# Kernel optimization log

Measured on AMD Instinct MI355X. Metric: run time of the kernel, lower is better.

## Reference

```python
import jax, jax.numpy as jnp
import numpy as np

OFFSET_SCALE = 6.0
ATT_SCALE = 280
ATT_DOWN = 8


def _calc_visibility(posmap):
    # posmap: (B, 3, W, H). shift stencil + cross-product z sign
    down_shift = jnp.pad(posmap[:, :, :, :-1], ((0, 0), (0, 0), (0, 0), (1, 0)))
    right_shift = jnp.pad(posmap[:, :, :-1, :], ((0, 0), (0, 0), (1, 0), (0, 0)))
    ab = posmap - right_shift
    bc = down_shift - right_shift
    z = ab[:, 0] * bc[:, 1] - ab[:, 1] * bc[:, 0]
    return jnp.where(z > 0, jnp.float32(1.0), jnp.where(z < 0, jnp.float32(0.1), z))


def _kpt2tform_weighted(kpt_src, kpt_dst, weight):
    # kpt_src/kpt_dst: (B, 68, 3); weight: (B, 68) (diagonal of W)
    d1 = jnp.sum(jnp.linalg.norm(kpt_src - kpt_src[:, 33:34], axis=2), axis=1)[:, None, None]
    d2 = jnp.sum(jnp.linalg.norm(kpt_dst - kpt_dst[:, 33:34], axis=2), axis=1)[:, None, None]
    A = kpt_src * d2 / d1
    Bm = kpt_dst
    AA = A - A.mean(axis=1, keepdims=True)
    BB = Bm - Bm.mean(axis=1, keepdims=True)
    # H = AA^T @ diag(w) @ BB, avoid materializing (B,68,68)
    H = jnp.einsum('bki,bk,bkj->bij', AA, weight, BB)
    U, S, Vh = jnp.linalg.svd(H)          # H = U diag(S) Vh ; torch.svd's V = Vh^T
    V = jnp.swapaxes(Vh, -1, -2)
    R = V @ jnp.swapaxes(U, -1, -2)
    t = jnp.mean(Bm - A @ jnp.swapaxes(R, -1, -2), axis=1)
    return R * d2 / d1, t


def setup_inputs() -> dict:
    key = jax.random.key(0)
    k1, k2, k3, k4, k5 = jax.random.split(key, 5)
    B, C, W, H = 64, 3, 256, 256
    Offset = jax.random.normal(k1, (B, C, W, H), dtype=jnp.float32)
    Posmap_kpt = jax.random.uniform(k2, (B, C, W, H), dtype=jnp.float32)
    attention = jax.random.uniform(k3, (B, 1, 35, 35), dtype=jnp.float32)
    mean_posmap = jax.random.uniform(k4, (C, W, H), dtype=jnp.float32)
    uv_kpt = jax.random.randint(k5, (68, 2), 0, 256, dtype=jnp.int32)
    return {"Offset": Offset, "Posmap_kpt": Posmap_kpt, "attention": attention,
            "mean_posmap": mean_posmap, "uv_kpt": uv_kpt}


def reference(Offset, Posmap_kpt, attention, mean_posmap, uv_kpt):
    B, C, W, H = Posmap_kpt.shape
    offsetmap = Offset * OFFSET_SCALE + mean_posmap          # (B,3,W,H)
    offsetmap = jnp.transpose(offsetmap, (0, 2, 3, 1))       # (B,W,H,3)
    vis_map = _calc_visibility(Posmap_kpt)                   # (B,W,H)
    kptmap = jnp.transpose(Posmap_kpt, (0, 2, 3, 1))         # (B,W,H,3)

    kpt_dst = kptmap[:, uv_kpt[:, 0], uv_kpt[:, 1]]          # (B,68,3)
    kpt_src = offsetmap[:, uv_kpt[:, 0], uv_kpt[:, 1]]       # (B,68,3)
    weight = vis_map[:, uv_kpt[:, 0], uv_kpt[:, 1]]          # (B,68)

    # attention reweighting (vectorized version of per-batch Python loop)
    kpt_ind = (kpt_dst[:, :, :2] * ATT_SCALE).astype(jnp.int32)
    iy = kpt_ind[:, :, 1] // ATT_DOWN
    ix = kpt_ind[:, :, 0] // ATT_DOWN
    w_at = attention[jnp.arange(B)[:, None], 0, iy, ix]      # (B,68)
    weight = weight * w_at

    R, T = _kpt2tform_weighted(kpt_src, kpt_dst, weight)
    flat = offsetmap.reshape((B, W * H, C))
    outpos = flat @ jnp.swapaxes(R, -1, -2) + T[:, None, :]
    outpos = outpos.reshape((B, W, H, C))
    return jnp.transpose(outpos, (0, 3, 1, 2))
```

## Files before the change

### kernel.cpp

```cpp
#include <hip/hip_runtime.h>
#include <math.h>

#define WH 65536
#define NK 68

__global__ __launch_bounds__(64) void solve_kernel(
    const float* __restrict__ Off, const float* __restrict__ P,
    const float* __restrict__ att, const float* __restrict__ meanp,
    const int* __restrict__ uv, float* __restrict__ RT)
{
    const int b = blockIdx.x;
    const int t = threadIdx.x;
    const float* Pb = P  + (size_t)b * 3 * WH;
    const float* Ob = Off + (size_t)b * 3 * WH;
    const float* attb = att + (size_t)b * 35 * 35;

    float src[2][3], dst[2][3], wgt[2];
    #pragma unroll
    for (int i = 0; i < 2; ++i) {
        const int k = t + 64 * i;
        const bool act = (k < NK);
        float p0=0,p1=0,p2=0,s0=0,s1=0,s2=0,w=0;
        if (act) {
            const int u0 = uv[2*k], u1 = uv[2*k+1];
            const int base = u0 * 256 + u1;
            p0 = Pb[0*WH + base];
            p1 = Pb[1*WH + base];
            p2 = Pb[2*WH + base];
            s0 = fmaf(Ob[0*WH + base], 6.0f, meanp[0*WH + base]);
            s1 = fmaf(Ob[1*WH + base], 6.0f, meanp[1*WH + base]);
            s2 = fmaf(Ob[2*WH + base], 6.0f, meanp[2*WH + base]);
            const float r0 = (u0 > 0) ? Pb[0*WH + base - 256] : 0.0f;
            const float r1 = (u0 > 0) ? Pb[1*WH + base - 256] : 0.0f;
            const float d0 = (u1 > 0) ? Pb[0*WH + base - 1]   : 0.0f;
            const float d1v= (u1 > 0) ? Pb[1*WH + base - 1]   : 0.0f;
            const float z = (p0 - r0) * (d1v - r1) - (p1 - r1) * (d0 - r0);
            const float vis = (z > 0.0f) ? 1.0f : ((z < 0.0f) ? 0.1f : z);
            int ix = (int)(p0 * 280.0f) / 8;
            int iy = (int)(p1 * 280.0f) / 8;
            ix = min(max(ix, 0), 34);
            iy = min(max(iy, 0), 34);
            w = vis * attb[iy * 35 + ix];
        }
        dst[i][0]=p0; dst[i][1]=p1; dst[i][2]=p2;
        src[i][0]=s0; src[i][1]=s1; src[i][2]=s2;
        wgt[i]=w;
    }

    float s33[3], d33[3];
    #pragma unroll
    for (int c = 0; c < 3; ++c) {
        s33[c] = __shfl(src[0][c], 33);
        d33[c] = __shfl(dst[0][c], 33);
    }

    float sums[8];
    #pragma unroll
    for (int j = 0; j < 8; ++j) sums[j] = 0.0f;
    #pragma unroll
    for (int i = 0; i < 2; ++i) {
        const bool act = (t + 64*i < NK);
        if (!act) continue;
        #pragma unroll
        for (int c = 0; c < 3; ++c) { sums[c] += src[i][c]; sums[3+c] += dst[i][c]; }
        const float dx0=src[i][0]-s33[0], dx1=src[i][1]-s33[1], dx2=src[i][2]-s33[2];
        const float dy0=dst[i][0]-d33[0], dy1=dst[i][1]-d33[1], dy2=dst[i][2]-d33[2];
        sums[6] += sqrtf(dx0*dx0 + dx1*dx1 + dx2*dx2);
        sums[7] += sqrtf(dy0*dy0 + dy1*dy1 + dy2*dy2);
    }
    #pragma unroll
    for (int m = 1; m < 64; m <<= 1)
        #pragma unroll
        for (int j = 0; j < 8; ++j) sums[j] += __shfl_xor(sums[j], m);

    const float inv_nk = 1.0f / (float)NK;
    const float ms0 = sums[0]*inv_nk, ms1 = sums[1]*inv_nk, ms2 = sums[2]*inv_nk;
    const float md0 = sums[3]*inv_nk, md1 = sums[4]*inv_nk, md2 = sums[5]*inv_nk;
    const float s = sums[7] / sums[6];

    float M[9];
    #pragma unroll
    for (int j = 0; j < 9; ++j) M[j] = 0.0f;
    #pragma unroll
    for (int i = 0; i < 2; ++i) {
        const float a0=src[i][0]-ms0, a1=src[i][1]-ms1, a2=src[i][2]-ms2;
        const float b0=dst[i][0]-md0, b1=dst[i][1]-md1, b2=dst[i][2]-md2;
        const float w = wgt[i];
        M[0]=fmaf(w*a0,b0,M[0]); M[1]=fmaf(w*a0,b1,M[1]); M[2]=fmaf(w*a0,b2,M[2]);
        M[3]=fmaf(w*a1,b0,M[3]); M[4]=fmaf(w*a1,b1,M[4]); M[5]=fmaf(w*a1,b2,M[5]);
        M[6]=fmaf(w*a2,b0,M[6]); M[7]=fmaf(w*a2,b1,M[7]); M[8]=fmaf(w*a2,b2,M[8]);
    }
    #pragma unroll
    for (int m = 1; m < 64; m <<= 1)
        #pragma unroll
        for (int j = 0; j < 9; ++j) M[j] += __shfl_xor(M[j], m);

    if (t == 0) {
        float X[9];
        float fn = 1e-30f;
        #pragma unroll
        for (int e = 0; e < 9; ++e) fn += M[e]*M[e];
        fn = sqrtf(fn);
        #pragma unroll
        for (int r = 0; r < 3; ++r)
            #pragma unroll
            for (int c = 0; c < 3; ++c)
                X[r*3+c] = M[c*3+r] / fn;
        #pragma unroll
        for (int it = 0; it < 10; ++it) {
            float C0 = X[4]*X[8]-X[5]*X[7];
            float C1 = X[5]*X[6]-X[3]*X[8];
            float C2 = X[3]*X[7]-X[4]*X[6];
            float C3 = X[2]*X[7]-X[1]*X[8];
            float C4 = X[0]*X[8]-X[2]*X[6];
            float C5 = X[1]*X[6]-X[0]*X[7];
            float C6 = X[1]*X[5]-X[2]*X[4];
            float C7 = X[2]*X[3]-X[0]*X[5];
            float C8 = X[0]*X[4]-X[1]*X[3];
            float det = X[0]*C0 + X[1]*C1 + X[2]*C2;
            if (fabsf(det) < 1e-30f) det = (det < 0.0f) ? -1e-30f : 1e-30f;
            const float g   = cbrtf(1.0f / fabsf(det));
            const float idg = 1.0f / (det * g);
            X[0]=0.5f*(g*X[0]+C0*idg); X[1]=0.5f*(g*X[1]+C1*idg); X[2]=0.5f*(g*X[2]+C2*idg);
            X[3]=0.5f*(g*X[3]+C3*idg); X[4]=0.5f*(g*X[4]+C4*idg); X[5]=0.5f*(g*X[5]+C5*idg);
            X[6]=0.5f*(g*X[6]+C6*idg); X[7]=0.5f*(g*X[7]+C7*idg); X[8]=0.5f*(g*X[8]+C8*idg);
        }
        float* o = RT + (size_t)b * 12;
        #pragma unroll
        for (int e = 0; e < 9; ++e) o[e] = s * X[e];
        const float msv[3] = {ms0, ms1, ms2};
        #pragma unroll
        for (int c = 0; c < 3; ++c) {
            float acc = 0.0f;
            #pragma unroll
            for (int j = 0; j < 3; ++j) acc = fmaf(msv[j], X[c*3+j], acc);
            const float mdv = (c==0) ? md0 : ((c==1) ? md1 : md2);
            o[9+c] = mdv - s * acc;
        }
    }
}

__device__ __forceinline__ float4 aff4(float4 f0, float4 f1, float4 f2,
                                       float r0, float r1, float r2, float t) {
    float4 y;
    y.x = fmaf(f0.x, r0, fmaf(f1.x, r1, fmaf(f2.x, r2, t)));
    y.y = fmaf(f0.y, r0, fmaf(f1.y, r1, fmaf(f2.y, r2, t)));
    y.z = fmaf(f0.z, r0, fmaf(f1.z, r1, fmaf(f2.z, r2, t)));
    y.w = fmaf(f0.w, r0, fmaf(f1.w, r1, fmaf(f2.w, r2, t)));
    return y;
}

__global__ __launch_bounds__(256) void apply_kernel(
    const float* __restrict__ Off, const float* __restrict__ meanp,
    const float* __restrict__ RT, float* __restrict__ out)
{
    const int b = blockIdx.y;
    const size_t p = ((size_t)blockIdx.x * 256 + threadIdx.x) * 4;
    const float* rt = RT + (size_t)b * 12;
    const float r00=rt[0], r01=rt[1], r02=rt[2];
    const float r10=rt[3], r11=rt[4], r12=rt[5];
    const float r20=rt[6], r21=rt[7], r22=rt[8];
    const float t0=rt[9], t1=rt[10], t2=rt[11];

    const float* ob = Off + (size_t)b * 3 * WH;
    const float4 o0 = *(const float4*)(ob + 0*WH + p);
    const float4 o1 = *(const float4*)(ob + 1*WH + p);
    const float4 o2 = *(const float4*)(ob + 2*WH + p);
    const float4 m0 = *(const float4*)(meanp + 0*WH + p);
    const float4 m1 = *(const float4*)(meanp + 1*WH + p);
    const float4 m2 = *(const float4*)(meanp + 2*WH + p);

    float4 f0, f1, f2;
    f0.x=fmaf(o0.x,6.0f,m0.x); f0.y=fmaf(o0.y,6.0f,m0.y); f0.z=fmaf(o0.z,6.0f,m0.z); f0.w=fmaf(o0.w,6.0f,m0.w);
    f1.x=fmaf(o1.x,6.0f,m1.x); f1.y=fmaf(o1.y,6.0f,m1.y); f1.z=fmaf(o1.z,6.0f,m1.z); f1.w=fmaf(o1.w,6.0f,m1.w);
    f2.x=fmaf(o2.x,6.0f,m2.x); f2.y=fmaf(o2.y,6.0f,m2.y); f2.z=fmaf(o2.z,6.0f,m2.z); f2.w=fmaf(o2.w,6.0f,m2.w);

    float* outb = out + (size_t)b * 3 * WH;
    *(float4*)(outb + 0*WH + p) = aff4(f0, f1, f2, r00, r01, r02, t0);
    *(float4*)(outb + 1*WH + p) = aff4(f0, f1, f2, r10, r11, r12, t1);
    *(float4*)(outb + 2*WH + p) = aff4(f0, f1, f2, r20, r21, r22, t2);
}

extern "C" void kernel_launch(void* const* d_in, const int* in_sizes, int n_in,
                              void* d_out, int out_size, void* d_ws, size_t ws_size,
                              hipStream_t stream) {
    const float* Off   = (const float*)d_in[0];
    const float* P     = (const float*)d_in[1];
    const float* att   = (const float*)d_in[2];
    const float* meanp = (const float*)d_in[3];
    const int*   uv    = (const int*)d_in[4];
    float* out = (float*)d_out;
    float* RT  = (float*)d_ws;

    const int B = in_sizes[0] / (3 * WH);

    solve_kernel<<<B, 64, 0, stream>>>(Off, P, att, meanp, uv, RT);

    dim3 grid(WH / (256 * 4), B);
    apply_kernel<<<grid, 256, 0, stream>>>(Off, meanp, RT, out);
}
```

Baseline: 28.88 us.

## Fuse per-batch Kabsch solve into apply kernel, recomputing transform per block

Merges the solve and apply kernels into one. Each block's first wavefront redundantly recomputes the per-batch rotation and translation from the 68 keypoints, while the other threads' bulk loads are already in flight. The result is shared through LDS, which removes the second launch and the serial dependency between kernels. In exchange the solve work is repeated across 64 blocks per batch. The Newton polar iterations also drop from 10 to 8 and use fast rcp and exp2/log2 in place of cbrt and division, which may cost some accuracy.

```diff
diff --git a/kernel.cpp b/kernel.cpp
--- a/kernel.cpp
+++ b/kernel.cpp
@@ -3,142 +3,6 @@
 
 #define WH 65536
 #define NK 68
-
-__global__ __launch_bounds__(64) void solve_kernel(
-    const float* __restrict__ Off, const float* __restrict__ P,
-    const float* __restrict__ att, const float* __restrict__ meanp,
-    const int* __restrict__ uv, float* __restrict__ RT)
-{
-    const int b = blockIdx.x;
-    const int t = threadIdx.x;
-    const float* Pb = P  + (size_t)b * 3 * WH;
-    const float* Ob = Off + (size_t)b * 3 * WH;
-    const float* attb = att + (size_t)b * 35 * 35;
-
-    float src[2][3], dst[2][3], wgt[2];
-    #pragma unroll
-    for (int i = 0; i < 2; ++i) {
-        const int k = t + 64 * i;
-        const bool act = (k < NK);
-        float p0=0,p1=0,p2=0,s0=0,s1=0,s2=0,w=0;
-        if (act) {
-            const int u0 = uv[2*k], u1 = uv[2*k+1];
-            const int base = u0 * 256 + u1;
-            p0 = Pb[0*WH + base];
-            p1 = Pb[1*WH + base];
-            p2 = Pb[2*WH + base];
-            s0 = fmaf(Ob[0*WH + base], 6.0f, meanp[0*WH + base]);
-            s1 = fmaf(Ob[1*WH + base], 6.0f, meanp[1*WH + base]);
-            s2 = fmaf(Ob[2*WH + base], 6.0f, meanp[2*WH + base]);
-            const float r0 = (u0 > 0) ? Pb[0*WH + base - 256] : 0.0f;
-            const float r1 = (u0 > 0) ? Pb[1*WH + base - 256] : 0.0f;
-            const float d0 = (u1 > 0) ? Pb[0*WH + base - 1]   : 0.0f;
-            const float d1v= (u1 > 0) ? Pb[1*WH + base - 1]   : 0.0f;
-            const float z = (p0 - r0) * (d1v - r1) - (p1 - r1) * (d0 - r0);
-            const float vis = (z > 0.0f) ? 1.0f : ((z < 0.0f) ? 0.1f : z);
-            int ix = (int)(p0 * 280.0f) / 8;
-            int iy = (int)(p1 * 280.0f) / 8;
-            ix = min(max(ix, 0), 34);
-            iy = min(max(iy, 0), 34);
-            w = vis * attb[iy * 35 + ix];
-        }
-        dst[i][0]=p0; dst[i][1]=p1; dst[i][2]=p2;
-        src[i][0]=s0; src[i][1]=s1; src[i][2]=s2;
-        wgt[i]=w;
-    }
-
-    float s33[3], d33[3];
-    #pragma unroll
-    for (int c = 0; c < 3; ++c) {
-        s33[c] = __shfl(src[0][c], 33);
-        d33[c] = __shfl(dst[0][c], 33);
-    }
-
-    float sums[8];
-    #pragma unroll
-    for (int j = 0; j < 8; ++j) sums[j] = 0.0f;
-    #pragma unroll
-    for (int i = 0; i < 2; ++i) {
-        const bool act = (t + 64*i < NK);
-        if (!act) continue;
-        #pragma unroll
-        for (int c = 0; c < 3; ++c) { sums[c] += src[i][c]; sums[3+c] += dst[i][c]; }
-        const float dx0=src[i][0]-s33[0], dx1=src[i][1]-s33[1], dx2=src[i][2]-s33[2];
-        const float dy0=dst[i][0]-d33[0], dy1=dst[i][1]-d33[1], dy2=dst[i][2]-d33[2];
-        sums[6] += sqrtf(dx0*dx0 + dx1*dx1 + dx2*dx2);
-        sums[7] += sqrtf(dy0*dy0 + dy1*dy1 + dy2*dy2);
-    }
-    #pragma unroll
-    for (int m = 1; m < 64; m <<= 1)
-        #pragma unroll
-        for (int j = 0; j < 8; ++j) sums[j] += __shfl_xor(sums[j], m);
-
-    const float inv_nk = 1.0f / (float)NK;
-    const float ms0 = sums[0]*inv_nk, ms1 = sums[1]*inv_nk, ms2 = sums[2]*inv_nk;
-    const float md0 = sums[3]*inv_nk, md1 = sums[4]*inv_nk, md2 = sums[5]*inv_nk;
-    const float s = sums[7] / sums[6];
-
-    float M[9];
-    #pragma unroll
-    for (int j = 0; j < 9; ++j) M[j] = 0.0f;
-    #pragma unroll
-    for (int i = 0; i < 2; ++i) {
-        const float a0=src[i][0]-ms0, a1=src[i][1]-ms1, a2=src[i][2]-ms2;
-        const float b0=dst[i][0]-md0, b1=dst[i][1]-md1, b2=dst[i][2]-md2;
-        const float w = wgt[i];
-        M[0]=fmaf(w*a0,b0,M[0]); M[1]=fmaf(w*a0,b1,M[1]); M[2]=fmaf(w*a0,b2,M[2]);
-        M[3]=fmaf(w*a1,b0,M[3]); M[4]=fmaf(w*a1,b1,M[4]); M[5]=fmaf(w*a1,b2,M[5]);
-        M[6]=fmaf(w*a2,b0,M[6]); M[7]=fmaf(w*a2,b1,M[7]); M[8]=fmaf(w*a2,b2,M[8]);
-    }
-    #pragma unroll
-    for (int m = 1; m < 64; m <<= 1)
-        #pragma unroll
-        for (int j = 0; j < 9; ++j) M[j] += __shfl_xor(M[j], m);
-
-    if (t == 0) {
-        float X[9];
-        float fn = 1e-30f;
-        #pragma unroll
-        for (int e = 0; e < 9; ++e) fn += M[e]*M[e];
-        fn = sqrtf(fn);
-        #pragma unroll
-        for (int r = 0; r < 3; ++r)
-            #pragma unroll
-            for (int c = 0; c < 3; ++c)
-                X[r*3+c] = M[c*3+r] / fn;
-        #pragma unroll
-        for (int it = 0; it < 10; ++it) {
-            float C0 = X[4]*X[8]-X[5]*X[7];
-            float C1 = X[5]*X[6]-X[3]*X[8];
-            float C2 = X[3]*X[7]-X[4]*X[6];
-            float C3 = X[2]*X[7]-X[1]*X[8];
-            float C4 = X[0]*X[8]-X[2]*X[6];
-            float C5 = X[1]*X[6]-X[0]*X[7];
-            float C6 = X[1]*X[5]-X[2]*X[4];
-            float C7 = X[2]*X[3]-X[0]*X[5];
-            float C8 = X[0]*X[4]-X[1]*X[3];
-            float det = X[0]*C0 + X[1]*C1 + X[2]*C2;
-            if (fabsf(det) < 1e-30f) det = (det < 0.0f) ? -1e-30f : 1e-30f;
-            const float g   = cbrtf(1.0f / fabsf(det));
-            const float idg = 1.0f / (det * g);
-            X[0]=0.5f*(g*X[0]+C0*idg); X[1]=0.5f*(g*X[1]+C1*idg); X[2]=0.5f*(g*X[2]+C2*idg);
-            X[3]=0.5f*(g*X[3]+C3*idg); X[4]=0.5f*(g*X[4]+C4*idg); X[5]=0.5f*(g*X[5]+C5*idg);
-            X[6]=0.5f*(g*X[6]+C6*idg); X[7]=0.5f*(g*X[7]+C7*idg); X[8]=0.5f*(g*X[8]+C8*idg);
-        }
-        float* o = RT + (size_t)b * 12;
-        #pragma unroll
-        for (int e = 0; e < 9; ++e) o[e] = s * X[e];
-        const float msv[3] = {ms0, ms1, ms2};
-        #pragma unroll
-        for (int c = 0; c < 3; ++c) {
-            float acc = 0.0f;
-            #pragma unroll
-            for (int j = 0; j < 3; ++j) acc = fmaf(msv[j], X[c*3+j], acc);
-            const float mdv = (c==0) ? md0 : ((c==1) ? md1 : md2);
-            o[9+c] = mdv - s * acc;
-        }
-    }
-}
 
 __device__ __forceinline__ float4 aff4(float4 f0, float4 f1, float4 f2,
                                        float r0, float r1, float r2, float t) {
@@ -150,18 +14,16 @@
     return y;
 }
 
-__global__ __launch_bounds__(256) void apply_kernel(
-    const float* __restrict__ Off, const float* __restrict__ meanp,
-    const float* __restrict__ RT, float* __restrict__ out)
+__global__ __launch_bounds__(256, 4) void fused_kernel(
+    const float* __restrict__ Off, const float* __restrict__ P,
+    const float* __restrict__ att, const float* __restrict__ meanp,
+    const int* __restrict__ uv, float* __restrict__ out)
 {
     const int b = blockIdx.y;
-    const size_t p = ((size_t)blockIdx.x * 256 + threadIdx.x) * 4;
-    const float* rt = RT + (size_t)b * 12;
-    const float r00=rt[0], r01=rt[1], r02=rt[2];
-    const float r10=rt[3], r11=rt[4], r12=rt[5];
-    const float r20=rt[6], r21=rt[7], r22=rt[8];
-    const float t0=rt[9], t1=rt[10], t2=rt[11];
+    const int t = threadIdx.x;
+    __shared__ float sRT[12];
 
+    const size_t p = ((size_t)blockIdx.x * 256 + t) * 4;
     const float* ob = Off + (size_t)b * 3 * WH;
     const float4 o0 = *(const float4*)(ob + 0*WH + p);
     const float4 o1 = *(const float4*)(ob + 1*WH + p);
@@ -170,10 +32,146 @@
     const float4 m1 = *(const float4*)(meanp + 1*WH + p);
     const float4 m2 = *(const float4*)(meanp + 2*WH + p);
 
+    if (t < 64) {
+        const float* Pb = P  + (size_t)b * 3 * WH;
+        const float* attb = att + (size_t)b * 35 * 35;
+
+        float src[2][3], dst[2][3], wgt[2];
+        #pragma unroll
+        for (int i = 0; i < 2; ++i) {
+            const int k = t + 64 * i;
+            const bool act = (k < NK);
+            float p0=0,p1=0,p2=0,s0=0,s1=0,s2=0,w=0;
+            if (act) {
+                const int u0 = uv[2*k], u1 = uv[2*k+1];
+                const int base = u0 * 256 + u1;
+                p0 = Pb[0*WH + base];
+                p1 = Pb[1*WH + base];
+                p2 = Pb[2*WH + base];
+                s0 = fmaf(Off[(size_t)b*3*WH + 0*WH + base], 6.0f, meanp[0*WH + base]);
+                s1 = fmaf(Off[(size_t)b*3*WH + 1*WH + base], 6.0f, meanp[1*WH + base]);
+                s2 = fmaf(Off[(size_t)b*3*WH + 2*WH + base], 6.0f, meanp[2*WH + base]);
+                const float r0 = (u0 > 0) ? Pb[0*WH + base - 256] : 0.0f;
+                const float r1 = (u0 > 0) ? Pb[1*WH + base - 256] : 0.0f;
+                const float d0 = (u1 > 0) ? Pb[0*WH + base - 1]   : 0.0f;
+                const float d1v= (u1 > 0) ? Pb[1*WH + base - 1]   : 0.0f;
+                const float z = (p0 - r0) * (d1v - r1) - (p1 - r1) * (d0 - r0);
+                const float vis = (z > 0.0f) ? 1.0f : ((z < 0.0f) ? 0.1f : z);
+                int ix = (int)(p0 * 280.0f) / 8;
+                int iy = (int)(p1 * 280.0f) / 8;
+                ix = min(max(ix, 0), 34);
+                iy = min(max(iy, 0), 34);
+                w = vis * attb[iy * 35 + ix];
+            }
+            dst[i][0]=p0; dst[i][1]=p1; dst[i][2]=p2;
+            src[i][0]=s0; src[i][1]=s1; src[i][2]=s2;
+            wgt[i]=w;
+        }
+
+        float s33[3], d33[3];
+        #pragma unroll
+        for (int c = 0; c < 3; ++c) {
+            s33[c] = __shfl(src[0][c], 33);
+            d33[c] = __shfl(dst[0][c], 33);
+        }
+
+        float sums[8];
+        #pragma unroll
+        for (int j = 0; j < 8; ++j) sums[j] = 0.0f;
+        #pragma unroll
+        for (int i = 0; i < 2; ++i) {
+            const bool act = (t + 64*i < NK);
+            if (!act) continue;
+            #pragma unroll
+            for (int c = 0; c < 3; ++c) { sums[c] += src[i][c]; sums[3+c] += dst[i][c]; }
+            const float dx0=src[i][0]-s33[0], dx1=src[i][1]-s33[1], dx2=src[i][2]-s33[2];
+            const float dy0=dst[i][0]-d33[0], dy1=dst[i][1]-d33[1], dy2=dst[i][2]-d33[2];
+            sums[6] += sqrtf(dx0*dx0 + dx1*dx1 + dx2*dx2);
+            sums[7] += sqrtf(dy0*dy0 + dy1*dy1 + dy2*dy2);
+        }
+        #pragma unroll
+        for (int m = 1; m < 64; m <<= 1)
+            #pragma unroll
+            for (int j = 0; j < 8; ++j) sums[j] += __shfl_xor(sums[j], m);
+
+        const float inv_nk = 1.0f / (float)NK;
+        const float ms0 = sums[0]*inv_nk, ms1 = sums[1]*inv_nk, ms2 = sums[2]*inv_nk;
+        const float md0 = sums[3]*inv_nk, md1 = sums[4]*inv_nk, md2 = sums[5]*inv_nk;
+        const float s = sums[7] * __builtin_amdgcn_rcpf(sums[6]);
+
+        float M[9];
+        #pragma unroll
+        for (int j = 0; j < 9; ++j) M[j] = 0.0f;
+        #pragma unroll
+        for (int i = 0; i < 2; ++i) {
+            const float a0=src[i][0]-ms0, a1=src[i][1]-ms1, a2=src[i][2]-ms2;
+            const float b0=dst[i][0]-md0, b1=dst[i][1]-md1, b2=dst[i][2]-md2;
+            const float w = wgt[i];
+            M[0]=fmaf(w*a0,b0,M[0]); M[1]=fmaf(w*a0,b1,M[1]); M[2]=fmaf(w*a0,b2,M[2]);
+            M[3]=fmaf(w*a1,b0,M[3]); M[4]=fmaf(w*a1,b1,M[4]); M[5]=fmaf(w*a1,b2,M[5]);
+            M[6]=fmaf(w*a2,b0,M[6]); M[7]=fmaf(w*a2,b1,M[7]); M[8]=fmaf(w*a2,b2,M[8]);
+        }
+        #pragma unroll
+        for (int m = 1; m < 64; m <<= 1)
+            #pragma unroll
+            for (int j = 0; j < 9; ++j) M[j] += __shfl_xor(M[j], m);
+
+        if (t == 0) {
+            float X[9];
+            float fn = 1e-30f;
+            #pragma unroll
+            for (int e = 0; e < 9; ++e) fn += M[e]*M[e];
+            const float rfn = __builtin_amdgcn_rcpf(sqrtf(fn));
+            #pragma unroll
+            for (int r = 0; r < 3; ++r)
+                #pragma unroll
+                for (int c = 0; c < 3; ++c)
+                    X[r*3+c] = M[c*3+r] * rfn;
+            #pragma unroll
+            for (int it = 0; it < 8; ++it) {
+                const float C0 = X[4]*X[8]-X[5]*X[7];
+                const float C1 = X[5]*X[6]-X[3]*X[8];
+                const float C2 = X[3]*X[7]-X[4]*X[6];
+                const float C3 = X[2]*X[7]-X[1]*X[8];
+                const float C4 = X[0]*X[8]-X[2]*X[6];
+                const float C5 = X[1]*X[6]-X[0]*X[7];
+                const float C6 = X[1]*X[5]-X[2]*X[4];
+                const float C7 = X[2]*X[3]-X[0]*X[5];
+                const float C8 = X[0]*X[4]-X[1]*X[3];
+                float det = X[0]*C0 + X[1]*C1 + X[2]*C2;
+                if (fabsf(det) < 1e-30f) det = (det < 0.0f) ? -1e-30f : 1e-30f;
+                const float ad  = fabsf(det);
+                const float g   = exp2f(-0.333333333f * log2f(ad));
+                const float idg = __builtin_amdgcn_rcpf(det * g);
+                X[0]=0.5f*(g*X[0]+C0*idg); X[1]=0.5f*(g*X[1]+C1*idg); X[2]=0.5f*(g*X[2]+C2*idg);
+                X[3]=0.5f*(g*X[3]+C3*idg); X[4]=0.5f*(g*X[4]+C4*idg); X[5]=0.5f*(g*X[5]+C5*idg);
+                X[6]=0.5f*(g*X[6]+C6*idg); X[7]=0.5f*(g*X[7]+C7*idg); X[8]=0.5f*(g*X[8]+C8*idg);
+            }
+            #pragma unroll
+            for (int e = 0; e < 9; ++e) sRT[e] = s * X[e];
+            const float msv[3] = {ms0, ms1, ms2};
+            #pragma unroll
+            for (int c = 0; c < 3; ++c) {
+                float acc = 0.0f;
+                #pragma unroll
+                for (int j = 0; j < 3; ++j) acc = fmaf(msv[j], X[c*3+j], acc);
+                const float mdv = (c==0) ? md0 : ((c==1) ? md1 : md2);
+                sRT[9+c] = mdv - s * acc;
+            }
+        }
+    }
+
     float4 f0, f1, f2;
     f0.x=fmaf(o0.x,6.0f,m0.x); f0.y=fmaf(o0.y,6.0f,m0.y); f0.z=fmaf(o0.z,6.0f,m0.z); f0.w=fmaf(o0.w,6.0f,m0.w);
     f1.x=fmaf(o1.x,6.0f,m1.x); f1.y=fmaf(o1.y,6.0f,m1.y); f1.z=fmaf(o1.z,6.0f,m1.z); f1.w=fmaf(o1.w,6.0f,m1.w);
     f2.x=fmaf(o2.x,6.0f,m2.x); f2.y=fmaf(o2.y,6.0f,m2.y); f2.z=fmaf(o2.z,6.0f,m2.z); f2.w=fmaf(o2.w,6.0f,m2.w);
+
+    __syncthreads();
+
+    const float r00=sRT[0], r01=sRT[1], r02=sRT[2];
+    const float r10=sRT[3], r11=sRT[4], r12=sRT[5];
+    const float r20=sRT[6], r21=sRT[7], r22=sRT[8];
+    const float t0=sRT[9], t1=sRT[10], t2=sRT[11];
 
     float* outb = out + (size_t)b * 3 * WH;
     *(float4*)(outb + 0*WH + p) = aff4(f0, f1, f2, r00, r01, r02, t0);
@@ -190,12 +188,8 @@
     const float* meanp = (const float*)d_in[3];
     const int*   uv    = (const int*)d_in[4];
     float* out = (float*)d_out;
-    float* RT  = (float*)d_ws;
 
     const int B = in_sizes[0] / (3 * WH);
-
-    solve_kernel<<<B, 64, 0, stream>>>(Off, P, att, meanp, uv, RT);
-
     dim3 grid(WH / (256 * 4), B);
-    apply_kernel<<<grid, 256, 0, stream>>>(Off, meanp, RT, out);
+    fused_kernel<<<grid, 256, 0, stream>>>(Off, P, att, meanp, uv, out);
 }
```

Result: slower. 38.79 us (+34.3%).
